# Optimization experiments

Hardware: AMD Instinct MI355X
Metric: run time of the kernel (lower is better)

Reference implementation:

```python
import jax, jax.numpy as jnp
import numpy as np

EPS = 1e-5
N_CONV = 3
B = 2048  # number of crystals


def _bn_eval(x, gamma, beta):
    # Eval-mode BatchNorm with running_mean=0, running_var=1.
    return x * (gamma / jnp.sqrt(1.0 + EPS)) + beta


def _conv_layer(atom_fea, nbr_fea, nbr_fea_idx, W, b, g1, b1, g2, b2):
    # Canonical CGCNN ConvLayer.
    N, M = nbr_fea_idx.shape
    F = atom_fea.shape[1]
    nbr_atom = atom_fea[nbr_fea_idx]                                  # [N,M,F]
    self_atom = jnp.broadcast_to(atom_fea[:, None, :], (N, M, F))     # [N,M,F]
    total = jnp.concatenate([self_atom, nbr_atom, nbr_fea], axis=2)   # [N,M,2F+nbr]
    gated = total @ W + b                                             # [N,M,2F]
    gated = _bn_eval(gated, g1, b1)
    flt, core = jnp.split(gated, 2, axis=2)
    nbr_sumed = jnp.sum(jax.nn.sigmoid(flt) * jax.nn.softplus(core), axis=1)  # [N,F]
    nbr_sumed = _bn_eval(nbr_sumed, g2, b2)
    return jax.nn.softplus(atom_fea + nbr_sumed)


def setup_inputs() -> dict:
    key = jax.random.key(0)
    ks = jax.random.split(key, 24)
    N, M = 60000, 12
    OA, NB, F, OE, E, H = 92, 41, 64, 8, 16, 128
    s = 0.05
    inp = {
        "atom_fea": jax.random.normal(ks[0], (N, OA), jnp.float32),
        "nbr_fea": jax.random.normal(ks[1], (N, M, NB), jnp.float32),
        "nbr_fea_idx": jax.random.randint(ks[2], (N, M), 0, N),
        "segment_ids": jnp.sort(jax.random.randint(ks[3], (N,), 0, B)),
        "extra_fea": jax.random.normal(ks[4], (B, OE), jnp.float32),
        # embedding_atom
        "W_embed": jax.random.normal(ks[5], (OA, F), jnp.float32) * s,
        "b_embed": jnp.zeros((F,), jnp.float32),
        # conv layers (stacked over n_conv=3)
        "conv_W": jax.random.normal(ks[6], (N_CONV, 2 * F + NB, 2 * F), jnp.float32) * s,
        "conv_b": jnp.zeros((N_CONV, 2 * F), jnp.float32),
        "bn1_g": jnp.ones((N_CONV, 2 * F), jnp.float32),
        "bn1_b": jnp.zeros((N_CONV, 2 * F), jnp.float32),
        "bn2_g": jnp.ones((N_CONV, F), jnp.float32),
        "bn2_b": jnp.zeros((N_CONV, F), jnp.float32),
        # embedding_extra
        "W_extra": jax.random.normal(ks[7], (OE, E), jnp.float32) * s,
        "b_extra": jnp.zeros((E,), jnp.float32),
        "bnx_g": jnp.ones((E,), jnp.float32),
        "bnx_b": jnp.zeros((E,), jnp.float32),
        # conv_to_fc
        "W_fc": jax.random.normal(ks[8], (F + E, H), jnp.float32) * s,
        "b_fc": jnp.zeros((H,), jnp.float32),
        "W_out0": jax.random.normal(ks[9], (H, 1), jnp.float32) * s,
        "b_out0": jnp.zeros((1,), jnp.float32),
        "W_out1": jax.random.normal(ks[10], (H, 2), jnp.float32) * s,
        "b_out1": jnp.zeros((2,), jnp.float32),
        "W_out2": jax.random.normal(ks[11], (H, 1), jnp.float32) * s,
        "b_out2": jnp.zeros((1,), jnp.float32),
    }
    return inp


def reference(atom_fea, nbr_fea, nbr_fea_idx, segment_ids, extra_fea,
              W_embed, b_embed, conv_W, conv_b, bn1_g, bn1_b, bn2_g, bn2_b,
              W_extra, b_extra, bnx_g, bnx_b, W_fc, b_fc,
              W_out0, b_out0, W_out1, b_out1, W_out2, b_out2):
    x = atom_fea @ W_embed + b_embed                                  # [N,F]
    extra = jax.nn.softplus(_bn_eval(extra_fea @ W_extra + b_extra, bnx_g, bnx_b))  # [B,E]
    for i in range(N_CONV):
        x = _conv_layer(x, nbr_fea, nbr_fea_idx, conv_W[i], conv_b[i],
                        bn1_g[i], bn1_b[i], bn2_g[i], bn2_b[i])
    # segment-mean pooling (replaces per-crystal python loop)
    sums = jax.ops.segment_sum(x, segment_ids, num_segments=B)        # [B,F]
    cnts = jax.ops.segment_sum(jnp.ones((x.shape[0],), x.dtype), segment_ids, num_segments=B)
    crys = sums / jnp.maximum(cnts, 1.0)[:, None]
    crys = jnp.concatenate([crys, extra], axis=1)                     # [B,F+E]
    crys = jax.nn.softplus(crys @ W_fc + b_fc)                        # [B,H]
    out0 = crys @ W_out0 + b_out0
    out1 = jax.nn.log_softmax(crys @ W_out1 + b_out1, axis=1)         # classification [B,2]
    out2 = crys @ W_out2 + b_out2
    return out0, out1, out2
```

## Files before the change

### kernel.cpp

```cpp
#include <hip/hip_runtime.h>
#include <math.h>
#include <stdint.h>

#define N_ATOMS 60000
#define M_NBR   12
#define NBF     41
#define B_CRYS  2048
#define EPSBN   1e-5f
#define GA      8
#define ROWS    (GA * M_NBR)
#define GRID_F  (N_ATOMS / GA)
#define WIMG_L  24576

typedef __attribute__((ext_vector_type(8))) short bf8;
typedef __attribute__((ext_vector_type(4))) float f32x4;
#define MFMA_B16(a, b, c) __builtin_amdgcn_mfma_f32_16x16x32_bf16(a, b, c, 0, 0, 0)

__device__ __forceinline__ short f2bf(float f) {
  uint32_t u = __builtin_bit_cast(uint32_t, f);
  u += 0x7FFFu + ((u >> 16) & 1u);
  return (short)(u >> 16);
}
__device__ __forceinline__ float lo16(uint32_t u) {
  return __builtin_bit_cast(float, u << 16);
}
__device__ __forceinline__ float hi16(uint32_t u) {
  return __builtin_bit_cast(float, u & 0xFFFF0000u);
}
__device__ __forceinline__ float sp(float x) {
  return (x > 15.f) ? x : __logf(1.f + __expf(x));
}
__device__ __forceinline__ float sig(float x) {
  return 1.f / (1.f + __expf(-x));
}

__global__ __launch_bounds__(256) void k_wprep(
    const float* __restrict__ conv_W, const float* __restrict__ conv_b,
    const float* __restrict__ bn1_g, const float* __restrict__ bn1_b,
    unsigned short* __restrict__ Wimg) {
  const int gid = blockIdx.x * 256 + threadIdx.x;
  if (gid >= 3 * WIMG_L) return;
  const int layer = gid / WIMG_L, rem = gid % WIMG_L;
  const int which = rem / 8192, r2 = rem % 8192;
  const int frag = r2 >> 9, lane = (r2 >> 3) & 63, j = r2 & 7;
  const int ct = frag >> 1, ks = frag & 1;
  const int quad = lane >> 4, l15 = lane & 15;
  const int jc = ct * 16 + l15;
  const int oc = (jc & 1) ? (jc >> 1) + 64 : (jc >> 1);
  const float s = bn1_g[layer * 128 + oc] * rsqrtf(1.f + EPSBN);
  const int k = ks * 32 + quad * 8 + j;
  const float* Wc = conv_W + (size_t)layer * 169 * 128;
  float v = 0.f;
  if (which == 0) {
    if (k < NBF) v = Wc[(128 + k) * 128 + oc] * s;
    else if (k == NBF) v = conv_b[layer * 128 + oc] * s + bn1_b[layer * 128 + oc];
  } else if (which == 1) {
    v = Wc[k * 128 + oc] * s;
  } else {
    v = Wc[(64 + k) * 128 + oc] * s;
  }
  Wimg[gid] = (unsigned short)f2bf(v);
}

__global__ __launch_bounds__(256) void k_embed2(
    const float* __restrict__ A, const float* __restrict__ W,
    const float* __restrict__ bias, float* __restrict__ X,
    unsigned int* __restrict__ XbU) {
  const int lane = threadIdx.x & 63, wv = threadIdx.x >> 6;
  const int quad = lane >> 4, l15 = lane & 15;
  const int gw = blockIdx.x * 4 + wv, nw = gridDim.x * 4;
  bf8 Bf[3][4];
  float bs[4];
#pragma unroll
  for (int ct = 0; ct < 4; ++ct) {
    const int col = ct * 16 + l15;
    bs[ct] = bias[col];
#pragma unroll
    for (int ks = 0; ks < 3; ++ks) {
      bf8 b;
#pragma unroll
      for (int i = 0; i < 8; ++i) {
        const int k = ks * 32 + quad * 8 + i;
        b[i] = (k < 92) ? f2bf(W[k * 64 + col]) : (short)0;
      }
      Bf[ks][ct] = b;
    }
  }
  for (int rt = gw; rt < 3750; rt += nw) {
    const int rbase = rt * 16;
    const float* ar = A + (size_t)(rbase + l15) * 92;
    const float4 p0 = *(const float4*)(ar + quad * 8);
    const float4 p1 = *(const float4*)(ar + quad * 8 + 4);
    const float4 p2 = *(const float4*)(ar + 32 + quad * 8);
    const float4 p3 = *(const float4*)(ar + 32 + quad * 8 + 4);
    bf8 A0, A1, A2;
    A0[0] = f2bf(p0.x); A0[1] = f2bf(p0.y); A0[2] = f2bf(p0.z); A0[3] = f2bf(p0.w);
    A0[4] = f2bf(p1.x); A0[5] = f2bf(p1.y); A0[6] = f2bf(p1.z); A0[7] = f2bf(p1.w);
    A1[0] = f2bf(p2.x); A1[1] = f2bf(p2.y); A1[2] = f2bf(p2.z); A1[3] = f2bf(p2.w);
    A1[4] = f2bf(p3.x); A1[5] = f2bf(p3.y); A1[6] = f2bf(p3.z); A1[7] = f2bf(p3.w);
#pragma unroll
    for (int i = 0; i < 8; ++i) {
      const int k = 64 + quad * 8 + i;
      A2[i] = (k < 92) ? f2bf(ar[k]) : (short)0;
    }
    const f32x4 z = {0.f, 0.f, 0.f, 0.f};
    f32x4 acc[4];
#pragma unroll
    for (int ct = 0; ct < 4; ++ct) {
      acc[ct] = MFMA_B16(A0, Bf[0][ct], z);
      acc[ct] = MFMA_B16(A1, Bf[1][ct], acc[ct]);
      acc[ct] = MFMA_B16(A2, Bf[2][ct], acc[ct]);
    }
#pragma unroll
    for (int ct = 0; ct < 4; ++ct)
#pragma unroll
      for (int r = 0; r < 4; ++r) {
        const int row = rbase + quad * 4 + r;
        const float v = acc[ct][r] + bs[ct];
        X[(size_t)row * 64 + ct * 16 + l15] = v;
        const unsigned int u = (unsigned short)f2bf(v);
        const unsigned int p = __shfl_xor((int)u, 1);
        if (!(l15 & 1))
          XbU[(size_t)row * 32 + ct * 8 + (l15 >> 1)] = u | (p << 16);
      }
  }
}

__global__ __launch_bounds__(256, 5) void k_fused4(
    float* __restrict__ X, const unsigned short* __restrict__ XbIn,
    unsigned int* __restrict__ XbOutU, const float* __restrict__ NF,
    const int* __restrict__ IDX, const unsigned short* __restrict__ Wi,
    const float* __restrict__ g2, const float* __restrict__ b2) {
  __shared__ __align__(16) unsigned int eb32[ROWS * 64];
  unsigned short* eb16 = (unsigned short*)eb32;
  float* stage = (float*)eb32;
  const int tid = threadIdx.x;
  const int lane = tid & 63, wv = tid >> 6;
  const int quad = lane >> 4, l15 = lane & 15;
  const int g = blockIdx.x;
  const int ntile = (wv < 2) ? 2 : 1;

  bf8 Ax0[2], Ax1[2], As0[2], As1[2];
#pragma unroll
  for (int ti = 0; ti < 2; ++ti) {
    if (ti < ntile) {
      const int rbase = (wv + ti * 4) * 16;
      const int jr = IDX[g * ROWS + rbase + l15];
      const unsigned short* xr = XbIn + (size_t)jr * 64 + quad * 8;
      Ax0[ti] = *(const bf8*)xr;
      Ax1[ti] = *(const bf8*)(xr + 32);
      const int arow = g * GA + (rbase + l15) / M_NBR;
      const unsigned short* sr = XbIn + (size_t)arow * 64 + quad * 8;
      As0[ti] = *(const bf8*)sr;
      As1[ti] = *(const bf8*)(sr + 32);
    }
  }

  const float4* s4 = (const float4*)(NF + (size_t)g * (ROWS * NBF));
#pragma unroll
  for (int it = 0; it < 4; ++it) {
    const int w = tid + it * 256;
    if (w < (ROWS * NBF) / 4) ((float4*)stage)[w] = s4[w];
  }
  __syncthreads();

  bf8 Ae0[2], Ae1[2];
#pragma unroll
  for (int ti = 0; ti < 2; ++ti) {
    if (ti < ntile) {
      const int rbase = (wv + ti * 4) * 16;
      const float* rp = stage + (rbase + l15) * NBF;
      bf8 a0, a1;
#pragma unroll
      for (int i = 0; i < 8; ++i) a0[i] = f2bf(rp[quad * 8 + i]);
      if (quad == 0) {
#pragma unroll
        for (int i = 0; i < 8; ++i) a1[i] = f2bf(rp[32 + i]);
      } else if (quad == 1) {
        a1[0] = f2bf(rp[40]);
        a1[1] = (short)0x3F80;
#pragma unroll
        for (int i = 2; i < 8; ++i) a1[i] = 0;
      } else {
#pragma unroll
        for (int i = 0; i < 8; ++i) a1[i] = 0;
      }
      Ae0[ti] = a0;
      Ae1[ti] = a1;
    }
  }
  __syncthreads();

#pragma unroll
  for (int ti = 0; ti < 2; ++ti) {
    if (ti < ntile) {
      const int rbase = (wv + ti * 4) * 16;
      const f32x4 z = {0.f, 0.f, 0.f, 0.f};
#pragma unroll 1
      for (int ct = 0; ct < 8; ++ct) {
        const bf8 Be0 = *(const bf8*)(Wi + ((ct * 2 + 0) * 64 + lane) * 8);
        const bf8 Be1 = *(const bf8*)(Wi + ((ct * 2 + 1) * 64 + lane) * 8);
        const bf8 Bs0 =
            *(const bf8*)(Wi + 8192 + ((ct * 2 + 0) * 64 + lane) * 8);
        const bf8 Bs1 =
            *(const bf8*)(Wi + 8192 + ((ct * 2 + 1) * 64 + lane) * 8);
        const bf8 Bn0 =
            *(const bf8*)(Wi + 16384 + ((ct * 2 + 0) * 64 + lane) * 8);
        const bf8 Bn1 =
            *(const bf8*)(Wi + 16384 + ((ct * 2 + 1) * 64 + lane) * 8);
        f32x4 acc = MFMA_B16(Ax0[ti], Bn0, z);
        acc = MFMA_B16(Ax1[ti], Bn1, acc);
        acc = MFMA_B16(As0[ti], Bs0, acc);
        acc = MFMA_B16(As1[ti], Bs1, acc);
        acc = MFMA_B16(Ae0[ti], Be0, acc);
        acc = MFMA_B16(Ae1[ti], Be1, acc);
        const int j = ct * 16 + l15;
        const int c = j >> 1, h = j & 1;
#pragma unroll
        for (int r = 0; r < 4; ++r) {
          const int row = rbase + quad * 4 + r;
          eb16[row * 128 + ((c + row) & 63) * 2 + h] =
              (unsigned short)f2bf(acc[r]);
        }
      }
    }
  }
  __syncthreads();

  const float inv = rsqrtf(1.f + EPSBN);
  const float s2 = g2[lane] * inv, o2 = b2[lane];
#pragma unroll
  for (int al = 0; al < 2; ++al) {
    const int a_local = wv * 2 + al;
    const int n = g * GA + a_local;
    float acc = 0.f;
#pragma unroll
    for (int m = 0; m < 12; ++m) {
      const int row = a_local * 12 + m;
      const uint32_t eu = eb32[row * 64 + ((lane + row) & 63)];
      acc += sig(lo16(eu)) * sp(hi16(eu));
    }
    const size_t o = (size_t)n * 64 + lane;
    const float res = sp(X[o] + acc * s2 + o2);
    X[o] = res;
    const unsigned int u = (unsigned short)f2bf(res);
    const unsigned int p = __shfl_xor((int)u, 1);
    if (!(lane & 1)) XbOutU[(size_t)n * 32 + (lane >> 1)] = u | (p << 16);
  }
}

__device__ __forceinline__ int lbound(const int* __restrict__ a, int n, int v) {
  int lo = 0, hi = n;
  while (lo < hi) {
    int mid = (lo + hi) >> 1;
    if (a[mid] < v) lo = mid + 1; else hi = mid;
  }
  return lo;
}

__global__ __launch_bounds__(128) void k_head(
    const float* __restrict__ Xf, const int* __restrict__ seg,
    const float* __restrict__ EF, const float* __restrict__ Wx,
    const float* __restrict__ bx, const float* __restrict__ gx,
    const float* __restrict__ bxb, const float* __restrict__ Wfc,
    const float* __restrict__ bfc, const float* __restrict__ Wo0,
    const float* __restrict__ bo0, const float* __restrict__ Wo1,
    const float* __restrict__ bo1, const float* __restrict__ Wo2,
    const float* __restrict__ bo2, float* __restrict__ out) {
  const int b = blockIdx.x;
  const int t = threadIdx.x;
  __shared__ float vbuf[80];
  __shared__ float part[128];
  __shared__ float4 r4[128];
  const int lo = lbound(seg, N_ATOMS, b);
  const int hi = lbound(seg, N_ATOMS, b + 1);
  const int col = t & 63, half = t >> 6;
  float s = 0.f;
  for (int r = lo + half; r < hi; r += 2) s += Xf[(size_t)r * 64 + col];
  part[t] = s;
  __syncthreads();
  if (t < 64) {
    vbuf[t] = (part[t] + part[t + 64]) / fmaxf((float)(hi - lo), 1.f);
  } else if (t < 80) {
    const int e = t - 64;
    float a = bx[e];
#pragma unroll
    for (int k = 0; k < 8; ++k) a += EF[b * 8 + k] * Wx[k * 16 + e];
    a = a * (gx[e] * rsqrtf(1.f + EPSBN)) + bxb[e];
    vbuf[t] = sp(a);
  }
  __syncthreads();
  float h = bfc[t];
#pragma unroll
  for (int k = 0; k < 80; ++k) h += vbuf[k] * Wfc[k * 128 + t];
  h = sp(h);
  r4[t] = make_float4(h * Wo0[t], h * Wo1[2 * t], h * Wo1[2 * t + 1],
                      h * Wo2[t]);
  __syncthreads();
  for (int st2 = 64; st2 > 0; st2 >>= 1) {
    if (t < st2) {
      float4 a = r4[t], c = r4[t + st2];
      r4[t] = make_float4(a.x + c.x, a.y + c.y, a.z + c.z, a.w + c.w);
    }
    __syncthreads();
  }
  if (t == 0) {
    float4 r = r4[0];
    out[b] = r.x + bo0[0];
    float z0 = r.y + bo1[0], z1 = r.z + bo1[1];
    float mx = fmaxf(z0, z1);
    float lse = mx + __logf(__expf(z0 - mx) + __expf(z1 - mx));
    out[B_CRYS + 2 * b] = z0 - lse;
    out[B_CRYS + 2 * b + 1] = z1 - lse;
    out[3 * B_CRYS + b] = r.w + bo2[0];
  }
}

extern "C" void kernel_launch(void* const* d_in, const int* in_sizes, int n_in,
                              void* d_out, int out_size, void* d_ws,
                              size_t ws_size, hipStream_t stream) {
  const float* atom_fea = (const float*)d_in[0];
  const float* nbr_fea  = (const float*)d_in[1];
  const int*   nbr_idx  = (const int*)d_in[2];
  const int*   seg      = (const int*)d_in[3];
  const float* extra    = (const float*)d_in[4];
  const float* W_embed  = (const float*)d_in[5];
  const float* b_embed  = (const float*)d_in[6];
  const float* conv_W   = (const float*)d_in[7];
  const float* conv_b   = (const float*)d_in[8];
  const float* bn1_g    = (const float*)d_in[9];
  const float* bn1_b    = (const float*)d_in[10];
  const float* bn2_g    = (const float*)d_in[11];
  const float* bn2_b    = (const float*)d_in[12];
  const float* W_extra  = (const float*)d_in[13];
  const float* b_extra  = (const float*)d_in[14];
  const float* bnx_g    = (const float*)d_in[15];
  const float* bnx_b    = (const float*)d_in[16];
  const float* W_fc     = (const float*)d_in[17];
  const float* b_fc     = (const float*)d_in[18];
  const float* W_out0   = (const float*)d_in[19];
  const float* b_out0   = (const float*)d_in[20];
  const float* W_out1   = (const float*)d_in[21];
  const float* b_out1   = (const float*)d_in[22];
  const float* W_out2   = (const float*)d_in[23];
  const float* b_out2   = (const float*)d_in[24];
  float* out = (float*)d_out;

  float* x = (float*)d_ws;
  unsigned int* xbu0 = (unsigned int*)(x + (size_t)N_ATOMS * 64);
  unsigned int* xbu1 = xbu0 + (size_t)N_ATOMS * 32;
  unsigned short* Wimg = (unsigned short*)(xbu1 + (size_t)N_ATOMS * 32);

  hipLaunchKernelGGL(k_wprep, dim3((3 * WIMG_L) / 256), dim3(256), 0, stream,
                     conv_W, conv_b, bn1_g, bn1_b, Wimg);
  hipLaunchKernelGGL(k_embed2, dim3(960), dim3(256), 0, stream, atom_fea,
                     W_embed, b_embed, x, xbu0);
  unsigned int* xin = xbu0;
  unsigned int* xout = xbu1;
  for (int i = 0; i < 3; ++i) {
    hipLaunchKernelGGL(k_fused4, dim3(GRID_F), dim3(256), 0, stream, x,
                       (const unsigned short*)xin, xout, nbr_fea, nbr_idx,
                       Wimg + (size_t)i * WIMG_L, bn2_g + i * 64,
                       bn2_b + i * 64);
    unsigned int* tmp = xin;
    xin = xout;
    xout = tmp;
  }
  hipLaunchKernelGGL(k_head, dim3(B_CRYS), dim3(128), 0, stream, x, seg, extra,
                     W_extra, b_extra, bnx_g, bnx_b, W_fc, b_fc, W_out0, b_out0,
                     W_out1, b_out1, W_out2, b_out2, out);
}
```

Baseline: 567.3 us.

## Pre-convert neighbor features to padded bf16 image once, read directly into MFMA operands

Adds a prep kernel that converts nbr_fea to a bf16 image padded to 48 columns, with a ones column folding in the bias, once per call. A new fused conv kernel loads these bf16 fragments straight from global memory into MFMA A operands, skipping per-layer fp32 staging and conversion in shared memory. This halves per-layer neighbor-feature bytes but adds an extra pass and workspace, and falls back to the old kernel if the workspace is too small.

```diff
diff --git a/kernel.cpp b/kernel.cpp
--- a/kernel.cpp
+++ b/kernel.cpp
@@ -11,6 +11,7 @@
 #define ROWS    (GA * M_NBR)
 #define GRID_F  (N_ATOMS / GA)
 #define WIMG_L  24576
+#define EROW    48
 
 typedef __attribute__((ext_vector_type(8))) short bf8;
 typedef __attribute__((ext_vector_type(4))) float f32x4;
@@ -62,6 +63,39 @@
   Wimg[gid] = (unsigned short)f2bf(v);
 }
 
+__global__ __launch_bounds__(256) void k_eprep(
+    const float* __restrict__ NF, unsigned short* __restrict__ Eimg) {
+  __shared__ __align__(16) float stage[ROWS * NBF];
+  const int tid = threadIdx.x;
+  const int g = blockIdx.x;
+  const float4* s4 = (const float4*)(NF + (size_t)g * (ROWS * NBF));
+#pragma unroll
+  for (int it = 0; it < 4; ++it) {
+    const int w = tid + it * 256;
+    if (w < (ROWS * NBF) / 4) ((float4*)stage)[w] = s4[w];
+  }
+  __syncthreads();
+#pragma unroll
+  for (int it = 0; it < 3; ++it) {
+    const int w = tid + it * 256;
+    if (w < (ROWS * EROW) / 8) {
+      const int row = w / 6, sg = w % 6, k0 = sg * 8;
+      const float* rp = stage + row * NBF;
+      bf8 v;
+#pragma unroll
+      for (int i = 0; i < 8; ++i) {
+        const int k = k0 + i;
+        short s;
+        if (k < NBF) s = f2bf(rp[k]);
+        else if (k == NBF) s = (short)0x3F80;
+        else s = 0;
+        v[i] = s;
+      }
+      *(bf8*)(Eimg + ((size_t)g * ROWS + row) * EROW + k0) = v;
+    }
+  }
+}
+
 __global__ __launch_bounds__(256) void k_embed2(
     const float* __restrict__ A, const float* __restrict__ W,
     const float* __restrict__ bias, float* __restrict__ X,
@@ -123,6 +157,101 @@
         if (!(l15 & 1))
           XbU[(size_t)row * 32 + ct * 8 + (l15 >> 1)] = u | (p << 16);
       }
+  }
+}
+
+__global__ __launch_bounds__(256, 5) void k_fused6(
+    float* __restrict__ X, const unsigned short* __restrict__ XbIn,
+    unsigned int* __restrict__ XbOutU, const unsigned short* __restrict__ Eimg,
+    const int* __restrict__ IDX, const unsigned short* __restrict__ Wi,
+    const float* __restrict__ g2, const float* __restrict__ b2) {
+  __shared__ __align__(16) unsigned int eb32[ROWS * 64];
+  unsigned short* eb16 = (unsigned short*)eb32;
+  const int tid = threadIdx.x;
+  const int lane = tid & 63, wv = tid >> 6;
+  const int quad = lane >> 4, l15 = lane & 15;
+  const int g = blockIdx.x;
+  const int ntile = (wv < 2) ? 2 : 1;
+
+  bf8 Ax0[2], Ax1[2], As0[2], As1[2], Ae0[2], Ae1[2];
+#pragma unroll
+  for (int ti = 0; ti < 2; ++ti) {
+    if (ti < ntile) {
+      const int rbase = (wv + ti * 4) * 16;
+      const int er = g * ROWS + rbase + l15;
+      const int jr = IDX[er];
+      const unsigned short* xr = XbIn + (size_t)jr * 64 + quad * 8;
+      Ax0[ti] = *(const bf8*)xr;
+      Ax1[ti] = *(const bf8*)(xr + 32);
+      const int arow = g * GA + (rbase + l15) / M_NBR;
+      const unsigned short* sr = XbIn + (size_t)arow * 64 + quad * 8;
+      As0[ti] = *(const bf8*)sr;
+      As1[ti] = *(const bf8*)(sr + 32);
+      const unsigned short* ep = Eimg + (size_t)er * EROW;
+      Ae0[ti] = *(const bf8*)(ep + quad * 8);
+      bf8 a1;
+#pragma unroll
+      for (int i = 0; i < 8; ++i) a1[i] = 0;
+      if (quad < 2) a1 = *(const bf8*)(ep + 32 + quad * 8);
+      Ae1[ti] = a1;
+    }
+  }
+
+#pragma unroll
+  for (int ti = 0; ti < 2; ++ti) {
+    if (ti < ntile) {
+      const int rbase = (wv + ti * 4) * 16;
+      const f32x4 z = {0.f, 0.f, 0.f, 0.f};
+#pragma unroll 1
+      for (int ct = 0; ct < 8; ++ct) {
+        const bf8 Be0 = *(const bf8*)(Wi + ((ct * 2 + 0) * 64 + lane) * 8);
+        const bf8 Be1 = *(const bf8*)(Wi + ((ct * 2 + 1) * 64 + lane) * 8);
+        const bf8 Bs0 =
+            *(const bf8*)(Wi + 8192 + ((ct * 2 + 0) * 64 + lane) * 8);
+        const bf8 Bs1 =
+            *(const bf8*)(Wi + 8192 + ((ct * 2 + 1) * 64 + lane) * 8);
+        const bf8 Bn0 =
+            *(const bf8*)(Wi + 16384 + ((ct * 2 + 0) * 64 + lane) * 8);
+        const bf8 Bn1 =
+            *(const bf8*)(Wi + 16384 + ((ct * 2 + 1) * 64 + lane) * 8);
+        f32x4 acc = MFMA_B16(Ax0[ti], Bn0, z);
+        acc = MFMA_B16(Ax1[ti], Bn1, acc);
+        acc = MFMA_B16(As0[ti], Bs0, acc);
+        acc = MFMA_B16(As1[ti], Bs1, acc);
+        acc = MFMA_B16(Ae0[ti], Be0, acc);
+        acc = MFMA_B16(Ae1[ti], Be1, acc);
+        const int j = ct * 16 + l15;
+        const int c = j >> 1, h = j & 1;
+#pragma unroll
+        for (int r = 0; r < 4; ++r) {
+          const int row = rbase + quad * 4 + r;
+          eb16[row * 128 + ((c + row) & 63) * 2 + h] =
+              (unsigned short)f2bf(acc[r]);
+        }
+      }
+    }
+  }
+  __syncthreads();
+
+  const float inv = rsqrtf(1.f + EPSBN);
+  const float s2 = g2[lane] * inv, o2 = b2[lane];
+#pragma unroll
+  for (int al = 0; al < 2; ++al) {
+    const int a_local = wv * 2 + al;
+    const int n = g * GA + a_local;
+    float acc = 0.f;
+#pragma unroll
+    for (int m = 0; m < 12; ++m) {
+      const int row = a_local * 12 + m;
+      const uint32_t eu = eb32[row * 64 + ((lane + row) & 63)];
+      acc += sig(lo16(eu)) * sp(hi16(eu));
+    }
+    const size_t o = (size_t)n * 64 + lane;
+    const float res = sp(X[o] + acc * s2 + o2);
+    X[o] = res;
+    const unsigned int u = (unsigned short)f2bf(res);
+    const unsigned int p = __shfl_xor((int)u, 1);
+    if (!(lane & 1)) XbOutU[(size_t)n * 32 + (lane >> 1)] = u | (p << 16);
   }
 }
 
@@ -350,18 +479,36 @@
   unsigned int* xbu0 = (unsigned int*)(x + (size_t)N_ATOMS * 64);
   unsigned int* xbu1 = xbu0 + (size_t)N_ATOMS * 32;
   unsigned short* Wimg = (unsigned short*)(xbu1 + (size_t)N_ATOMS * 32);
+  unsigned short* Eimg = Wimg + (size_t)3 * WIMG_L;
+
+  const size_t base_bytes =
+      (size_t)N_ATOMS * 64 * 4 + (size_t)N_ATOMS * 32 * 4 * 2 +
+      (size_t)3 * WIMG_L * 2;
+  const size_t eimg_bytes = (size_t)GRID_F * ROWS * EROW * 2;
+  const bool use_eimg = (ws_size >= base_bytes + eimg_bytes);
 
   hipLaunchKernelGGL(k_wprep, dim3((3 * WIMG_L) / 256), dim3(256), 0, stream,
                      conv_W, conv_b, bn1_g, bn1_b, Wimg);
+  if (use_eimg) {
+    hipLaunchKernelGGL(k_eprep, dim3(GRID_F), dim3(256), 0, stream, nbr_fea,
+                       Eimg);
+  }
   hipLaunchKernelGGL(k_embed2, dim3(960), dim3(256), 0, stream, atom_fea,
                      W_embed, b_embed, x, xbu0);
   unsigned int* xin = xbu0;
   unsigned int* xout = xbu1;
   for (int i = 0; i < 3; ++i) {
-    hipLaunchKernelGGL(k_fused4, dim3(GRID_F), dim3(256), 0, stream, x,
-                       (const unsigned short*)xin, xout, nbr_fea, nbr_idx,
-                       Wimg + (size_t)i * WIMG_L, bn2_g + i * 64,
-                       bn2_b + i * 64);
+    if (use_eimg) {
+      hipLaunchKernelGGL(k_fused6, dim3(GRID_F), dim3(256), 0, stream, x,
+                         (const unsigned short*)xin, xout, Eimg, nbr_idx,
+                         Wimg + (size_t)i * WIMG_L, bn2_g + i * 64,
+                         bn2_b + i * 64);
+    } else {
+      hipLaunchKernelGGL(k_fused4, dim3(GRID_F), dim3(256), 0, stream, x,
+                         (const unsigned short*)xin, xout, nbr_fea, nbr_idx,
+                         Wimg + (size_t)i * WIMG_L, bn2_g + i * 64,
+                         bn2_b + i * 64);
+    }
     unsigned int* tmp = xin;
     xin = xout;
     xout = tmp;
```

Result: no change. 565.9 us (-0.2%).
